# Performance work log

Measured on AMD Instinct MI355X. Metric: run time of the kernel, lower is better.

The kernel has to match this reference:

```python
import jax, jax.numpy as jnp
import numpy as np

B, D_IN, D_HID, D_OUT = 1024, 4096, 4096, 2048
SPARSITY = 50
K_PR = int(SPARSITY * 1.5)        # sparsity * sparsity_boost = 75
K_SHIFT = SPARSITY + 1            # int(sparsity + 1) = 51
SUM_NORM = 1.0
GAIN = 2.0
EPS = 1e-13


def topk_mask(y, k):
    """1.0 at the top-k entries of each row (dim=1), else 0.0 (= build_topk_mask)."""
    _, idx = jax.lax.top_k(y, k)                      # [B, k]
    rows = jnp.arange(y.shape[0])[:, None]
    return jnp.zeros_like(y).at[rows, idx].set(1.0)


def setup_inputs() -> dict:
    key = jax.random.key(0)
    k0, k1, k2, k3 = jax.random.split(key, 4)
    inputs = jax.random.uniform(k0, (B, D_IN), dtype=jnp.float32)
    targets = jax.random.uniform(k1, (B, D_OUT), dtype=jnp.float32)  # BCE targets in [0,1]
    s1 = float(1.0 / np.sqrt(D_IN))
    s2 = float(1.0 / np.sqrt(D_HID))
    w_enc = jax.random.uniform(k2, (D_IN, D_HID), jnp.float32, -s1, s1)
    b_enc = jnp.zeros((D_HID,), jnp.float32)
    w_dec = jax.random.uniform(k3, (D_HID, D_OUT), jnp.float32, -s2, s2)
    b_dec = jnp.zeros((D_OUT,), jnp.float32)
    return {"inputs": inputs, "targets": targets, "w_enc": w_enc, "b_enc": b_enc,
            "w_dec": w_dec, "b_dec": b_dec}


def reference(inputs, targets, w_enc, b_enc, w_dec, b_dec):
    # SimpleAutoencoder forward: encoder Linear + nonlinearity, decoder Linear -> logits
    hidden = jax.nn.leaky_relu(inputs @ w_enc + b_enc)          # [B, D_HID]
    logits = hidden @ w_dec + b_dec                             # [B, D_OUT]

    # F.binary_cross_entropy_with_logits, mean reduction (numerically stable)
    loss = jnp.mean(jnp.maximum(logits, 0.0) - logits * targets
                    + jnp.log1p(jnp.exp(-jnp.abs(logits))))

    # post-hoc chain (detached in torch; forward math identical)
    y = jax.nn.sigmoid(logits)
    y = jnp.clip(y, 0.0, 1.0)
    # sparsen
    y = y * topk_mask(y, K_PR)
    # sum_norm > 0
    y_sum = jnp.sum(y, axis=1, keepdims=True)
    y = y * (1.0 / y_sum + EPS) * SUM_NORM
    # softmax (torch F.softmax default dim=1 for 2D)
    y = jax.nn.softmax(y, axis=1)
    # gain
    y = y * GAIN
    pr_out = y

    # shift_range: unit -> [-1, 1]
    z_cue_in = pr_out * 2.0 - 1.0

    # shift_bits: get_pc_topk_shift(pr_out, sparsity)
    cue_mask = topk_mask(pr_out, K_SHIFT)
    y_inv_masked_max = jnp.max((1.0 - pr_out) * cue_mask, axis=1)   # [B]
    y_masked_min = 1.0 - y_inv_masked_max
    cue_tanh_masked_min = y_masked_min * 2.0 - 1.0
    shift = (0.0 - cue_tanh_masked_min)[:, None]                    # [B, 1]
    z_cue = z_cue_in + shift

    return (loss, pr_out, z_cue_in, z_cue)
```

## Files before the change

### kernel.cpp

```cpp
#include <hip/hip_runtime.h>
#include <hip/hip_bf16.h>


typedef unsigned short u16;
typedef unsigned int u32;
typedef __attribute__((ext_vector_type(4))) float f32x4;
typedef __attribute__((ext_vector_type(8))) short s16x8;

#define GAS __attribute__((address_space(1)))
#define LAS __attribute__((address_space(3)))

__device__ __forceinline__ u16 f2bf(float x) {
  u32 u = __float_as_uint(x);
  u32 r = (u + 0x7FFFu + ((u >> 16) & 1u)) >> 16;
  return (u16)r;
}

__device__ __forceinline__ void gld_lds16(const u16* g, u16* l) {
  __builtin_amdgcn_global_load_lds((const GAS void*)g, (LAS void*)l, 16, 0, 0);
}


__global__ void cast_bf16_kernel(const float* __restrict__ in,
                                 u16* __restrict__ out, int n4) {
  int i = blockIdx.x * 256 + threadIdx.x;
  if (i < n4) {
    float4 v = ((const float4*)in)[i];
    u32 p0 = (u32)f2bf(v.x) | ((u32)f2bf(v.y) << 16);
    u32 p1 = (u32)f2bf(v.z) | ((u32)f2bf(v.w) << 16);
    uint2 p; p.x = p0; p.y = p1;
    ((uint2*)out)[i] = p;
  }
}

__global__ __launch_bounds__(256) void tcast_kernel(const float* __restrict__ in,
                                                    u16* __restrict__ out,
                                                    int R, int C) {
  __shared__ float tile[32][33];
  const int cb = blockIdx.x * 32, rb = blockIdx.y * 32;
  const int tx = threadIdx.x, ty = threadIdx.y;
#pragma unroll
  for (int i = 0; i < 4; i++)
    tile[ty + i * 8][tx] = in[(size_t)(rb + ty + i * 8) * C + cb + tx];
  __syncthreads();
#pragma unroll
  for (int i = 0; i < 4; i++)
    out[(size_t)(cb + ty + i * 8) * R + rb + tx] = f2bf(tile[tx][ty + i * 8]);
}


template <int ACT>
__global__ __launch_bounds__(256, 2) void gemm2ph_kernel(
    const u16* __restrict__ A, const u16* __restrict__ BT,
    const float* __restrict__ bias, void* __restrict__ out,
    int M, int N, int K, int klen) {
  constexpr int BM = 128, BN = 128, BK = 64;
  constexpr int MF = 4, NF = 4;
  constexpr int BUF = BM * BK + BN * BK;
  __shared__ __align__(16) u16 smem[2 * BUF];

  const int tid = threadIdx.x;
  const int wid = tid >> 6, lane = tid & 63;
  const int wm = wid >> 1, wn = wid & 1;
  const int n0 = blockIdx.x * BN, m0 = blockIdx.y * BM;
  const int kbase = blockIdx.z * klen;

  f32x4 acc[MF][NF];
#pragma unroll
  for (int f = 0; f < MF; f++)
#pragma unroll
    for (int j = 0; j < NF; j++) acc[f][j] = (f32x4)0.f;

  const u16* Ag = A + (size_t)(m0 + (lane >> 3)) * K + kbase + (lane & 7) * 8;
  const u16* Bg = BT + (size_t)(n0 + (lane >> 3)) * K + kbase + (lane & 7) * 8;
  const int fr = lane & 15, fg = lane >> 4;
  const int NT = klen / BK;

  auto stage = [&](int b, int koff) {
    u16* Al = smem + b * BUF;
    u16* Bl = Al + BM * BK;
#pragma unroll
    for (int t2 = 0; t2 < 4; t2++) {
      const int i = wid * 4 + t2;
      gld_lds16(Ag + (size_t)i * 8 * K + koff, Al + i * 512);
      gld_lds16(Bg + (size_t)i * 8 * K + koff, Bl + i * 512);
    }
  };

  stage(0, 0);
  __syncthreads();
  int cur = 0;
  for (int t = 0; t < NT; t++) {
    if (t + 1 < NT) stage(cur ^ 1, (t + 1) * BK);

    const u16* Ab = smem + cur * BUF;
    const u16* Bb = Ab + BM * BK;
    s16x8 af[MF][2], bf[NF][2];
#pragma unroll
    for (int f = 0; f < MF; f++)
#pragma unroll
      for (int kk = 0; kk < 2; kk++)
        af[f][kk] = *(const s16x8*)&Ab[(wm * 64 + f * 16 + fr) * BK + kk * 32 + fg * 8];
#pragma unroll
    for (int j = 0; j < NF; j++)
#pragma unroll
      for (int kk = 0; kk < 2; kk++)
        bf[j][kk] = *(const s16x8*)&Bb[(wn * 64 + j * 16 + fr) * BK + kk * 32 + fg * 8];
#pragma unroll
    for (int kk = 0; kk < 2; kk++)
#pragma unroll
      for (int f = 0; f < MF; f++)
#pragma unroll
        for (int j = 0; j < NF; j++)
          acc[f][j] = __builtin_amdgcn_mfma_f32_16x16x32_bf16(
              af[f][kk], bf[j][kk], acc[f][j], 0, 0, 0);

    __syncthreads();
    cur ^= 1;
  }

#pragma unroll
  for (int j = 0; j < NF; j++) {
    const int col = n0 + wn * 64 + j * 16 + fr;
    const float bv = ACT ? bias[col] : 0.f;
#pragma unroll
    for (int f = 0; f < MF; f++) {
#pragma unroll
      for (int q = 0; q < 4; q++) {
        const int row = m0 + wm * 64 + f * 16 + fg * 4 + q;
        if (ACT) {
          float v = acc[f][j][q] + bv;
          v = (v > 0.f) ? v : 0.01f * v;
          ((u16*)out)[(size_t)row * N + col] = f2bf(v);
        } else {
          float* o = (float*)out + (size_t)blockIdx.z * M * N;
          o[(size_t)row * N + col] = acc[f][j][q];
        }
      }
    }
  }
}


__device__ __forceinline__ float wred_sum(float v) {
#pragma unroll
  for (int o = 32; o; o >>= 1) v += __shfl_xor(v, o, 64);
  return v;
}
__device__ __forceinline__ float wred_max(float v) {
#pragma unroll
  for (int o = 32; o; o >>= 1) v = fmaxf(v, __shfl_xor(v, o, 64));
  return v;
}
__device__ __forceinline__ u32 wred_sumu(u32 v) {
#pragma unroll
  for (int o = 32; o; o >>= 1) v += (u32)__shfl_xor((int)v, o, 64);
  return v;
}


__global__ __launch_bounds__(256) void epilogue_wave_kernel(
    const float* __restrict__ p0, const float* __restrict__ p1,
    const float* __restrict__ p2, const float* __restrict__ p3,
    const float* __restrict__ b_dec, const float* __restrict__ targets,
    float* __restrict__ out, float* __restrict__ lossp) {
  const int tid = threadIdx.x;
  const int widx = tid >> 6, lane = tid & 63;
  const int r = blockIdx.x * 4 + widx;
  const size_t base = (size_t)r * 2048 + lane * 32;

  u32 u[32];
  float bce = 0.f, ymax = 0.f;
#pragma unroll
  for (int g = 0; g < 8; g++) {
    float4 a = *(const float4*)(p0 + base + g * 4);
    float4 b = *(const float4*)(p1 + base + g * 4);
    float4 d = *(const float4*)(p2 + base + g * 4);
    float4 e = *(const float4*)(p3 + base + g * 4);
    float4 c4 = *(const float4*)(b_dec + lane * 32 + g * 4);
    float4 t4 = *(const float4*)(targets + base + g * 4);
    float lv[4] = {a.x + b.x + d.x + e.x + c4.x, a.y + b.y + d.y + e.y + c4.y,
                   a.z + b.z + d.z + e.z + c4.z, a.w + b.w + d.w + e.w + c4.w};
    float tv[4] = {t4.x, t4.y, t4.z, t4.w};
#pragma unroll
    for (int j = 0; j < 4; j++) {
      float li = lv[j];
      bce += fmaxf(li, 0.f) - li * tv[j] + log1pf(expf(-fabsf(li)));
      float yi = 1.f / (1.f + expf(-li));
      u[g * 4 + j] = __float_as_uint(yi);
      ymax = fmaxf(ymax, yi);
    }
  }
  bce = wred_sum(bce);
  if (lane == 0) lossp[r] = bce;
  ymax = wred_max(ymax);

  u32 T75 = 0, T51 = 0;
  for (int b = 29; b >= 0; b--) {
    const u32 c75 = T75 | (1u << b), c51 = T51 | (1u << b);
    u32 cnt = 0;
#pragma unroll
    for (int i = 0; i < 32; i++) {
      cnt += (u[i] >= c75) ? 1u : 0u;
      cnt += (u[i] >= c51) ? 0x10000u : 0u;
    }
    cnt = wred_sumu(cnt);
    if ((cnt & 0xFFFFu) >= 75u) T75 = c75;
    if ((cnt >> 16) >= 51u) T51 = c51;
  }

  u32 cc = 0; float sgt = 0.f;
#pragma unroll
  for (int i = 0; i < 32; i++) {
    if (u[i] > T75)       { cc += 1u; sgt += __uint_as_float(u[i]); }
    else if (u[i] == T75) { cc += 0x10000u; }
  }
  cc = wred_sumu(cc);
  sgt = wred_sum(sgt);
  const u32 G = cc & 0xFFFFu, E = cc >> 16;
  const u32 need = 75u - G;
  const float t75f = __uint_as_float(T75);
  const float ysum = sgt + (float)need * t75f;

  u32 selmask = 0;
#pragma unroll
  for (int i = 0; i < 32; i++)
    if (u[i] >= T75) selmask |= (1u << i);
  if (need != E) {
    u32 eqm = 0;
#pragma unroll
    for (int i = 0; i < 32; i++)
      if (u[i] == T75) eqm |= (1u << i);
    u32 eqc = __popc(eqm);
    u32 pre = eqc;
#pragma unroll
    for (int o = 1; o < 64; o <<= 1) {
      u32 t = (u32)__shfl_up((int)pre, o, 64);
      if (lane >= o) pre += t;
    }
    pre -= eqc;
    u32 m = eqm, rank = pre;
    while (m) {
      u32 i = (u32)__ffs(m) - 1u;
      m &= m - 1u;
      if (rank >= need) selmask &= ~(1u << i);
      rank++;
    }
  }

  const float c = 1.f / ysum + 1e-13f;
  const float Mv = c * ymax;
  float zs = 0.f;
#pragma unroll
  for (int i = 0; i < 32; i++) {
    float yi = __uint_as_float(u[i]);
    float v = ((selmask >> i) & 1u) ? c * yi : 0.f;
    float e = expf(v - Mv);
    zs += e;
    u[i] = __float_as_uint(e);
  }
  const float Z = wred_sum(zs);
  const float gZ = 2.f / Z;
  const float shift = 1.f - 2.f * (expf(c * __uint_as_float(T51) - Mv) * gZ);

  float* pr_o = out + 1;
  float* zi_o = out + 1 + 2097152;
  float* zc_o = out + 1 + 4194304;
#pragma unroll
  for (int i = 0; i < 32; i++) {
    float pr = __uint_as_float(u[i]) * gZ;
    float zi = 2.f * pr - 1.f;
    pr_o[base + i] = pr;
    zi_o[base + i] = zi;
    zc_o[base + i] = zi + shift;
  }
}

__global__ void loss_reduce_kernel(const float* __restrict__ lp,
                                   float* __restrict__ out) {
  const int tid = threadIdx.x;
  float s = 0.f;
  for (int i = tid; i < 1024; i += 256) s += lp[i];
  __shared__ float sf[4];
  float v = s;
#pragma unroll
  for (int o = 32; o; o >>= 1) v += __shfl_down(v, o, 64);
  if ((tid & 63) == 0) sf[tid >> 6] = v;
  __syncthreads();
  if (tid == 0) out[0] = (sf[0] + sf[1] + sf[2] + sf[3]) * (1.f / (1024.f * 2048.f));
}


extern "C" void kernel_launch(void* const* d_in, const int* in_sizes, int n_in,
                              void* d_out, int out_size, void* d_ws, size_t ws_size,
                              hipStream_t stream) {
  (void)in_sizes; (void)n_in; (void)out_size; (void)ws_size;
  const float* inputs  = (const float*)d_in[0];
  const float* targets = (const float*)d_in[1];
  const float* w_enc   = (const float*)d_in[2];
  const float* b_enc   = (const float*)d_in[3];
  const float* w_dec   = (const float*)d_in[4];
  const float* b_dec   = (const float*)d_in[5];
  float* out = (float*)d_out;

  char* ws = (char*)d_ws;
  u16* A16 = (u16*)ws;
  u16* W1T = (u16*)(ws + (8u << 20));
  u16* W2T = (u16*)(ws + (40u << 20));
  u16* H16 = (u16*)(ws + (56u << 20));
  float* lgts  = (float*)(ws + (8u << 20));
  float* lossp = (float*)ws;

  cast_bf16_kernel<<<4096, 256, 0, stream>>>(inputs, A16, 1024 * 4096 / 4);
  tcast_kernel<<<dim3(128, 128), dim3(32, 8), 0, stream>>>(w_enc, W1T, 4096, 4096);
  tcast_kernel<<<dim3(64, 128), dim3(32, 8), 0, stream>>>(w_dec, W2T, 4096, 2048);

  gemm2ph_kernel<1><<<dim3(32, 8), 256, 0, stream>>>(
      A16, W1T, b_enc, (void*)H16, 1024, 4096, 4096, 4096);
  gemm2ph_kernel<0><<<dim3(16, 8, 4), 256, 0, stream>>>(
      H16, W2T, nullptr, (void*)lgts, 1024, 2048, 4096, 1024);

  const float* q0 = lgts;
  const float* q1 = lgts + (size_t)2 * 1024 * 1024;
  const float* q2 = lgts + (size_t)4 * 1024 * 1024;
  const float* q3 = lgts + (size_t)6 * 1024 * 1024;
  epilogue_wave_kernel<<<256, 256, 0, stream>>>(q0, q1, q2, q3, b_dec,
                                                targets, out, lossp);
  loss_reduce_kernel<<<1, 256, 0, stream>>>(lossp, out);
}
```

Measured before the change: 320.5 us.

## Fuse prep casts into one kernel and coalesce epilogue row layout

Merges the input cast and the two weight transpose-casts into a single launch dispatched by block index, removing two kernel launches. The epilogue now assigns each lane strided float4 chunks (g*256 + lane*4) instead of a contiguous 32-element slab, so both loads and the three output streams are coalesced, and stores become float4. Tie-breaking at the top-k threshold is reworked to use wave ballots in the new element order rather than a shuffle prefix scan, which keeps first-index tie semantics under the changed layout.

```diff
diff --git a/kernel.cpp b/kernel.cpp
--- a/kernel.cpp
+++ b/kernel.cpp
@@ -4,6 +4,7 @@
 
 typedef unsigned short u16;
 typedef unsigned int u32;
+typedef unsigned long long u64;
 typedef __attribute__((ext_vector_type(4))) float f32x4;
 typedef __attribute__((ext_vector_type(8))) short s16x8;
 
@@ -21,24 +22,12 @@
 }
 
 
-__global__ void cast_bf16_kernel(const float* __restrict__ in,
-                                 u16* __restrict__ out, int n4) {
-  int i = blockIdx.x * 256 + threadIdx.x;
-  if (i < n4) {
-    float4 v = ((const float4*)in)[i];
-    u32 p0 = (u32)f2bf(v.x) | ((u32)f2bf(v.y) << 16);
-    u32 p1 = (u32)f2bf(v.z) | ((u32)f2bf(v.w) << 16);
-    uint2 p; p.x = p0; p.y = p1;
-    ((uint2*)out)[i] = p;
-  }
-}
-
-__global__ __launch_bounds__(256) void tcast_kernel(const float* __restrict__ in,
-                                                    u16* __restrict__ out,
-                                                    int R, int C) {
+__device__ __forceinline__ void tcast_body(const float* __restrict__ in,
+                                           u16* __restrict__ out, int R, int C,
+                                           int bx, int by, int tid) {
   __shared__ float tile[32][33];
-  const int cb = blockIdx.x * 32, rb = blockIdx.y * 32;
-  const int tx = threadIdx.x, ty = threadIdx.y;
+  const int cb = bx * 32, rb = by * 32;
+  const int tx = tid & 31, ty = tid >> 5;
 #pragma unroll
   for (int i = 0; i < 4; i++)
     tile[ty + i * 8][tx] = in[(size_t)(rb + ty + i * 8) * C + cb + tx];
@@ -46,6 +35,27 @@
 #pragma unroll
   for (int i = 0; i < 4; i++)
     out[(size_t)(cb + ty + i * 8) * R + rb + tx] = f2bf(tile[tx][ty + i * 8]);
+}
+
+__global__ __launch_bounds__(256) void prep_kernel(
+    const float* __restrict__ inputs, const float* __restrict__ w_enc,
+    const float* __restrict__ w_dec, u16* __restrict__ A16,
+    u16* __restrict__ W1T, u16* __restrict__ W2T) {
+  const int bid = blockIdx.x, tid = threadIdx.x;
+  if (bid < 4096) {
+    const int i = bid * 256 + tid;
+    float4 v = ((const float4*)inputs)[i];
+    uint2 p;
+    p.x = (u32)f2bf(v.x) | ((u32)f2bf(v.y) << 16);
+    p.y = (u32)f2bf(v.z) | ((u32)f2bf(v.w) << 16);
+    ((uint2*)A16)[i] = p;
+  } else if (bid < 20480) {
+    const int idx = bid - 4096;
+    tcast_body(w_enc, W1T, 4096, 4096, idx & 127, idx >> 7, tid);
+  } else {
+    const int idx = bid - 20480;
+    tcast_body(w_dec, W2T, 4096, 2048, idx & 63, idx >> 6, tid);
+  }
 }
 
 
@@ -167,18 +177,19 @@
   const int tid = threadIdx.x;
   const int widx = tid >> 6, lane = tid & 63;
   const int r = blockIdx.x * 4 + widx;
-  const size_t base = (size_t)r * 2048 + lane * 32;
+  const size_t rb = (size_t)r * 2048;
 
   u32 u[32];
   float bce = 0.f, ymax = 0.f;
 #pragma unroll
   for (int g = 0; g < 8; g++) {
-    float4 a = *(const float4*)(p0 + base + g * 4);
-    float4 b = *(const float4*)(p1 + base + g * 4);
-    float4 d = *(const float4*)(p2 + base + g * 4);
-    float4 e = *(const float4*)(p3 + base + g * 4);
-    float4 c4 = *(const float4*)(b_dec + lane * 32 + g * 4);
-    float4 t4 = *(const float4*)(targets + base + g * 4);
+    const size_t o = rb + g * 256 + lane * 4;
+    float4 a = *(const float4*)(p0 + o);
+    float4 b = *(const float4*)(p1 + o);
+    float4 d = *(const float4*)(p2 + o);
+    float4 e = *(const float4*)(p3 + o);
+    float4 c4 = *(const float4*)(b_dec + g * 256 + lane * 4);
+    float4 t4 = *(const float4*)(targets + o);
     float lv[4] = {a.x + b.x + d.x + e.x + c4.x, a.y + b.y + d.y + e.y + c4.y,
                    a.z + b.z + d.z + e.z + c4.z, a.w + b.w + d.w + e.w + c4.w};
     float tv[4] = {t4.x, t4.y, t4.z, t4.w};
@@ -227,24 +238,28 @@
   for (int i = 0; i < 32; i++)
     if (u[i] >= T75) selmask |= (1u << i);
   if (need != E) {
-    u32 eqm = 0;
-#pragma unroll
-    for (int i = 0; i < 32; i++)
-      if (u[i] == T75) eqm |= (1u << i);
-    u32 eqc = __popc(eqm);
-    u32 pre = eqc;
-#pragma unroll
-    for (int o = 1; o < 64; o <<= 1) {
-      u32 t = (u32)__shfl_up((int)pre, o, 64);
-      if (lane >= o) pre += t;
-    }
-    pre -= eqc;
-    u32 m = eqm, rank = pre;
-    while (m) {
-      u32 i = (u32)__ffs(m) - 1u;
-      m &= m - 1u;
-      if (rank >= need) selmask &= ~(1u << i);
-      rank++;
+    const u64 ltm = ((u64)1 << lane) - 1ull;
+    u32 cum = 0;
+#pragma unroll
+    for (int g = 0; g < 8; g++) {
+      u64 bm[4];
+      u32 below = 0, grp = 0;
+#pragma unroll
+      for (int j = 0; j < 4; j++) {
+        bm[j] = __ballot(u[g * 4 + j] == T75);
+        below += (u32)__popcll(bm[j] & ltm);
+        grp += (u32)__popcll(bm[j]);
+      }
+      u32 same = 0;
+#pragma unroll
+      for (int j = 0; j < 4; j++) {
+        const int r2 = g * 4 + j;
+        if (u[r2] == T75) {
+          if (cum + below + same >= need) selmask &= ~(1u << r2);
+          same++;
+        }
+      }
+      cum += grp;
     }
   }
 
@@ -267,12 +282,21 @@
   float* zi_o = out + 1 + 2097152;
   float* zc_o = out + 1 + 4194304;
 #pragma unroll
-  for (int i = 0; i < 32; i++) {
-    float pr = __uint_as_float(u[i]) * gZ;
-    float zi = 2.f * pr - 1.f;
-    pr_o[base + i] = pr;
-    zi_o[base + i] = zi;
-    zc_o[base + i] = zi + shift;
+  for (int g = 0; g < 8; g++) {
+    float4 pr4, zi4, zc4;
+    float e0 = __uint_as_float(u[g * 4 + 0]) * gZ;
+    float e1 = __uint_as_float(u[g * 4 + 1]) * gZ;
+    float e2 = __uint_as_float(u[g * 4 + 2]) * gZ;
+    float e3 = __uint_as_float(u[g * 4 + 3]) * gZ;
+    pr4 = make_float4(e0, e1, e2, e3);
+    zi4 = make_float4(2.f * e0 - 1.f, 2.f * e1 - 1.f, 2.f * e2 - 1.f,
+                      2.f * e3 - 1.f);
+    zc4 = make_float4(zi4.x + shift, zi4.y + shift, zi4.z + shift,
+                      zi4.w + shift);
+    const size_t o = rb + g * 256 + lane * 4;
+    *(float4*)(pr_o + o) = pr4;
+    *(float4*)(zi_o + o) = zi4;
+    *(float4*)(zc_o + o) = zc4;
   }
 }
 
@@ -311,9 +335,7 @@
   float* lgts  = (float*)(ws + (8u << 20));
   float* lossp = (float*)ws;
 
-  cast_bf16_kernel<<<4096, 256, 0, stream>>>(inputs, A16, 1024 * 4096 / 4);
-  tcast_kernel<<<dim3(128, 128), dim3(32, 8), 0, stream>>>(w_enc, W1T, 4096, 4096);
-  tcast_kernel<<<dim3(64, 128), dim3(32, 8), 0, stream>>>(w_dec, W2T, 4096, 2048);
+  prep_kernel<<<28672, 256, 0, stream>>>(inputs, w_enc, w_dec, A16, W1T, W2T);
 
   gemm2ph_kernel<1><<<dim3(32, 8), 256, 0, stream>>>(
       A16, W1T, b_enc, (void*)H16, 1024, 4096, 4096, 4096);
```

Result: faster. 289.0 us (-9.8%).
